# Kernel tuning notes

Measured on AMD Instinct MI355X. Metric: run time of the kernel, lower is better.

Reference implementation:

```python
import jax, jax.numpy as jnp
import numpy as np

N_IN = 100000
N_OUT = 200000
C_IN = 128
C_OUT = 64
K = 27  # 3x3x3 kernel offsets
M = 100000  # neighbor-map pairs per kernel offset
BN_EPS = 1e-5


def setup_inputs() -> dict:
    key = jax.random.key(0)
    k1, k2, k3, k4 = jax.random.split(key, 4)
    x = jax.random.normal(k1, (N_IN, C_IN), dtype=jnp.float32)
    weight = jax.random.normal(k2, (K, C_IN, C_OUT), dtype=jnp.float32) * (1.0 / np.sqrt(C_IN * K))
    gamma = jnp.ones((C_OUT,), dtype=jnp.float32)
    beta = jnp.zeros((C_OUT,), dtype=jnp.float32)
    in_map = jax.random.randint(k3, (K, M), 0, N_IN, dtype=jnp.int32)
    out_map = jax.random.randint(k4, (K, M), 0, N_OUT, dtype=jnp.int32)
    return {"x": x, "weight": weight, "gamma": gamma, "beta": beta,
            "in_map": in_map, "out_map": out_map}


def sparse_transposed_conv(x, weight, in_map, out_map):
    # gather-GEMM-scatter over K kernel offsets (torchsparse semantics)
    out = jnp.zeros((N_OUT, C_OUT), dtype=x.dtype)

    def body(k, out):
        gathered = x[in_map[k]]                # [M, C_in] irregular gather
        contrib = gathered @ weight[k]         # [M, C_out] small GEMM
        return out.at[out_map[k]].add(contrib) # irregular scatter-add

    return jax.lax.fori_loop(0, K, body, out)


def reference(x, weight, gamma, beta, in_map, out_map):
    out = sparse_transposed_conv(x, weight, in_map, out_map)
    # BatchNorm over points (training-mode batch statistics, biased var)
    mean = jnp.mean(out, axis=0)
    var = jnp.mean(jnp.square(out - mean), axis=0)
    y = (out - mean) * (gamma * jax.lax.rsqrt(var + BN_EPS)) + beta
    return jnp.maximum(y, 0.0)  # ReLU
```

## Files before the change

### kernel.cpp

```cpp
#include <hip/hip_runtime.h>
#include <hip/hip_fp16.h>

#define N_IN   100000
#define N_OUT  200000
#define C_IN   128
#define C_OUT  64
#define NK     27
#define MM     100000
#define BN_EPS 1e-5f

#define TILE_M 128
#define APAD   136

typedef short bf16x8 __attribute__((ext_vector_type(8)));
typedef float f32x4  __attribute__((ext_vector_type(4)));

__device__ __forceinline__ unsigned pack2_bf16(float a, float b) {
  unsigned ua = __float_as_uint(a);
  unsigned ub = __float_as_uint(b);
  ua = (ua + 0x7FFFu + ((ua >> 16) & 1u)) >> 16;
  ub = (ub + 0x7FFFu + ((ub >> 16) & 1u)) & 0xFFFF0000u;
  return ua | ub;
}

__device__ __forceinline__ unsigned pack2_f16(float lo, float hi) {
  __half2 h = __floats2half2_rn(lo, hi);
  return *(unsigned*)&h;
}

__device__ __forceinline__ void pk_atomic_f16(const void* addr, unsigned pw) {
  asm volatile("global_atomic_pk_add_f16 %0, %1, off"
               :: "v"((unsigned long long)addr), "v"(pw) : "memory");
}

__global__ void convert_kernel(const float* __restrict__ x, unsigned* __restrict__ xb,
                               const float* __restrict__ w, unsigned* __restrict__ wt) {
  if (blockIdx.x < 6250) {
    int id = blockIdx.x * 256 + threadIdx.x;
    const float4* xs = (const float4*)x;
    float4 v0 = xs[2 * id];
    float4 v1 = xs[2 * id + 1];
    uint4 o;
    o.x = pack2_bf16(v0.x, v0.y);
    o.y = pack2_bf16(v0.z, v0.w);
    o.z = pack2_bf16(v1.x, v1.y);
    o.w = pack2_bf16(v1.z, v1.w);
    ((uint4*)xb)[id] = o;
  } else {
    int pidx = (blockIdx.x - 6250) * 256 + threadIdx.x;
    int k   = pidx >> 12;
    int rem = pidx & 4095;
    int co  = rem >> 6;
    int ci0 = (rem & 63) * 2;
    const float* wk = w + (size_t)k * C_IN * C_OUT;
    float a = wk[ci0 * C_OUT + co];
    float b = wk[(ci0 + 1) * C_OUT + co];
    wt[pidx] = pack2_bf16(a, b);
  }
}

__global__ __launch_bounds__(256, 4) void scatter3_kernel(
    const uint4* __restrict__ xb,
    const unsigned short* __restrict__ wt,
    const int* __restrict__ in_map,
    const int* __restrict__ out_map,
    unsigned short* __restrict__ acc16)
{
  __shared__ unsigned short Bls[C_OUT * APAD];

  const int t = threadIdx.x;
  const int k = blockIdx.y;
  const int mbase = blockIdx.x * TILE_M;

  {
    const uint4* src = (const uint4*)(wt + (size_t)k * C_OUT * C_IN);
    #pragma unroll
    for (int i = 0; i < 4; ++i) {
      int ch  = t + i * 256;
      int co  = ch >> 4;
      int ci0 = (ch & 15) * 8;
      *(uint4*)&Bls[co * APAD + ci0] = src[ch];
    }
  }

  const int wave = t >> 6;
  const int lane = t & 63;
  const int quad = lane >> 4;
  const int l15  = lane & 15;
  const int rb   = wave * 32;

  const int m0 = mbase + rb + l15;
  const int m1 = m0 + 16;
  const int src0 = (m0 < MM) ? in_map[k * MM + m0] : 0;
  const int src1 = (m1 < MM) ? in_map[k * MM + m1] : 0;
  const uint4* xr0 = xb + (size_t)src0 * 16 + quad;
  const uint4* xr1 = xb + (size_t)src1 * 16 + quad;
  uint4 a0[4], a1[4];
  #pragma unroll
  for (int kk = 0; kk < 4; ++kk) {
    a0[kk] = xr0[kk * 4];
    a1[kk] = xr1[kk * 4];
  }

  __syncthreads();

  f32x4 acc[2][4];
  #pragma unroll
  for (int i = 0; i < 2; ++i)
    #pragma unroll
    for (int j = 0; j < 4; ++j)
      acc[i][j] = (f32x4){0.f, 0.f, 0.f, 0.f};

  #pragma unroll
  for (int kk = 0; kk < 4; ++kk) {
    const int koff = kk * 32 + quad * 8;
    bf16x8 fa0 = *(const bf16x8*)&a0[kk];
    bf16x8 fa1 = *(const bf16x8*)&a1[kk];
    bf16x8 b0 = *(const bf16x8*)&Bls[(l15) * APAD + koff];
    bf16x8 b1 = *(const bf16x8*)&Bls[(16 + l15) * APAD + koff];
    bf16x8 b2 = *(const bf16x8*)&Bls[(32 + l15) * APAD + koff];
    bf16x8 b3 = *(const bf16x8*)&Bls[(48 + l15) * APAD + koff];
    acc[0][0] = __builtin_amdgcn_mfma_f32_16x16x32_bf16(fa0, b0, acc[0][0], 0, 0, 0);
    acc[0][1] = __builtin_amdgcn_mfma_f32_16x16x32_bf16(fa0, b1, acc[0][1], 0, 0, 0);
    acc[0][2] = __builtin_amdgcn_mfma_f32_16x16x32_bf16(fa0, b2, acc[0][2], 0, 0, 0);
    acc[0][3] = __builtin_amdgcn_mfma_f32_16x16x32_bf16(fa0, b3, acc[0][3], 0, 0, 0);
    acc[1][0] = __builtin_amdgcn_mfma_f32_16x16x32_bf16(fa1, b0, acc[1][0], 0, 0, 0);
    acc[1][1] = __builtin_amdgcn_mfma_f32_16x16x32_bf16(fa1, b1, acc[1][1], 0, 0, 0);
    acc[1][2] = __builtin_amdgcn_mfma_f32_16x16x32_bf16(fa1, b2, acc[1][2], 0, 0, 0);
    acc[1][3] = __builtin_amdgcn_mfma_f32_16x16x32_bf16(fa1, b3, acc[1][3], 0, 0, 0);
  }

  const int par = l15 & 1;
  #pragma unroll
  for (int rt = 0; rt < 2; ++rt) {
    int rloc = rb + rt * 16 + quad * 4;
    int mrow = mbase + rloc;
    int4 o4;
    if (mrow + 3 < MM) {
      o4 = *(const int4*)(out_map + (size_t)k * MM + mrow);
    } else {
      o4.x = (mrow + 0 < MM) ? out_map[(size_t)k * MM + mrow + 0] : 0;
      o4.y = (mrow + 1 < MM) ? out_map[(size_t)k * MM + mrow + 1] : 0;
      o4.z = (mrow + 2 < MM) ? out_map[(size_t)k * MM + mrow + 2] : 0;
      o4.w = (mrow + 3 < MM) ? out_map[(size_t)k * MM + mrow + 3] : 0;
    }
    int om4[4] = {o4.x, o4.y, o4.z, o4.w};
    #pragma unroll
    for (int ct = 0; ct < 4; ++ct) {
      f32x4 v = acc[rt][ct];
      int colb = ct * 16 + (l15 & ~1);
      #pragma unroll
      for (int i = 0; i < 4; ++i) {
        float vn = __shfl_xor(v[i], 1);
        float lo = par ? vn : v[i];
        float hi = par ? v[i] : vn;
        unsigned pw = pack2_f16(lo, hi);
        if (((i & 1) == par) && (mrow + i < MM)) {
          const unsigned short* addr = acc16 + (size_t)om4[i] * C_OUT + colb;
          pk_atomic_f16(addr, pw);
        }
      }
    }
  }
}

__global__ __launch_bounds__(256) void scatter_f32_kernel(
    const float* __restrict__ x,
    const unsigned short* __restrict__ wt,
    const int* __restrict__ in_map,
    const int* __restrict__ out_map,
    float* __restrict__ outf)
{
  __shared__ unsigned short Als[TILE_M * APAD];
  __shared__ unsigned short Bls[C_OUT * APAD];
  __shared__ int om[TILE_M];

  const int t = threadIdx.x;
  const int k = blockIdx.y;
  const int mbase = blockIdx.x * TILE_M;

  if (t < TILE_M) {
    int m = mbase + t;
    om[t] = (m < MM) ? out_map[k * MM + m] : 0;
  }
  {
    const uint4* src = (const uint4*)(wt + (size_t)k * C_OUT * C_IN);
    #pragma unroll
    for (int i = 0; i < 4; ++i) {
      int ch  = t + i * 256;
      int co  = ch >> 4;
      int ci0 = (ch & 15) * 8;
      *(uint4*)&Bls[co * APAD + ci0] = src[ch];
    }
  }
  {
    int r    = t >> 1;
    int half = t & 1;
    int m    = mbase + r;
    int src  = (m < MM) ? in_map[k * MM + m] : 0;
    const float4* xr = (const float4*)(x + (size_t)src * C_IN) + half * 16;
    uint2* dst = (uint2*)&Als[r * APAD + half * 64];
    #pragma unroll
    for (int j = 0; j < 16; ++j) {
      float4 v = xr[j];
      dst[j] = make_uint2(pack2_bf16(v.x, v.y), pack2_bf16(v.z, v.w));
    }
  }
  __syncthreads();

  const int wave = t >> 6;
  const int lane = t & 63;
  const int quad = lane >> 4;
  const int l15  = lane & 15;
  const int rb   = wave * 32;

  f32x4 acc[2][4];
  #pragma unroll
  for (int i = 0; i < 2; ++i)
    #pragma unroll
    for (int j = 0; j < 4; ++j)
      acc[i][j] = (f32x4){0.f, 0.f, 0.f, 0.f};

  #pragma unroll
  for (int kk = 0; kk < 4; ++kk) {
    const int koff = kk * 32 + quad * 8;
    bf16x8 a0 = *(const bf16x8*)&Als[(rb + l15) * APAD + koff];
    bf16x8 a1 = *(const bf16x8*)&Als[(rb + 16 + l15) * APAD + koff];
    bf16x8 b0 = *(const bf16x8*)&Bls[(l15) * APAD + koff];
    bf16x8 b1 = *(const bf16x8*)&Bls[(16 + l15) * APAD + koff];
    bf16x8 b2 = *(const bf16x8*)&Bls[(32 + l15) * APAD + koff];
    bf16x8 b3 = *(const bf16x8*)&Bls[(48 + l15) * APAD + koff];
    acc[0][0] = __builtin_amdgcn_mfma_f32_16x16x32_bf16(a0, b0, acc[0][0], 0, 0, 0);
    acc[0][1] = __builtin_amdgcn_mfma_f32_16x16x32_bf16(a0, b1, acc[0][1], 0, 0, 0);
    acc[0][2] = __builtin_amdgcn_mfma_f32_16x16x32_bf16(a0, b2, acc[0][2], 0, 0, 0);
    acc[0][3] = __builtin_amdgcn_mfma_f32_16x16x32_bf16(a0, b3, acc[0][3], 0, 0, 0);
    acc[1][0] = __builtin_amdgcn_mfma_f32_16x16x32_bf16(a1, b0, acc[1][0], 0, 0, 0);
    acc[1][1] = __builtin_amdgcn_mfma_f32_16x16x32_bf16(a1, b1, acc[1][1], 0, 0, 0);
    acc[1][2] = __builtin_amdgcn_mfma_f32_16x16x32_bf16(a1, b2, acc[1][2], 0, 0, 0);
    acc[1][3] = __builtin_amdgcn_mfma_f32_16x16x32_bf16(a1, b3, acc[1][3], 0, 0, 0);
  }

  #pragma unroll
  for (int rt = 0; rt < 2; ++rt) {
    int rloc = rb + rt * 16 + quad * 4;
    int4 o4 = *(const int4*)&om[rloc];
    int mrow = mbase + rloc;
    #pragma unroll
    for (int ct = 0; ct < 4; ++ct) {
      f32x4 v = acc[rt][ct];
      int col = ct * 16 + l15;
      if (mrow + 0 < MM) unsafeAtomicAdd(&outf[(size_t)o4.x * C_OUT + col], v[0]);
      if (mrow + 1 < MM) unsafeAtomicAdd(&outf[(size_t)o4.y * C_OUT + col], v[1]);
      if (mrow + 2 < MM) unsafeAtomicAdd(&outf[(size_t)o4.z * C_OUT + col], v[2]);
      if (mrow + 3 < MM) unsafeAtomicAdd(&outf[(size_t)o4.w * C_OUT + col], v[3]);
    }
  }
}

__global__ __launch_bounds__(256) void stats16_kernel(const unsigned* __restrict__ acc,
                                                      float* __restrict__ ws) {
  __shared__ float red[4][8][32];
  int t = threadIdx.x;
  int w = t & 31, sub = t >> 5;
  float s0 = 0, q0 = 0, s1 = 0, q1 = 0;
  for (int r = blockIdx.x * 8 + sub; r < N_OUT; r += gridDim.x * 8) {
    unsigned u = acc[(size_t)r * 32 + w];
    __half2 h = *(__half2*)&u;
    float a = __low2float(h), b = __high2float(h);
    s0 += a; q0 += a * a; s1 += b; q1 += b * b;
  }
  red[0][sub][w] = s0; red[1][sub][w] = q0;
  red[2][sub][w] = s1; red[3][sub][w] = q1;
  __syncthreads();
  if (t < 32) {
    float S0 = 0, Q0 = 0, S1 = 0, Q1 = 0;
    #pragma unroll
    for (int s = 0; s < 8; ++s) {
      S0 += red[0][s][t]; Q0 += red[1][s][t];
      S1 += red[2][s][t]; Q1 += red[3][s][t];
    }
    unsafeAtomicAdd(&ws[2 * t],      S0);
    unsafeAtomicAdd(&ws[64 + 2 * t], Q0);
    unsafeAtomicAdd(&ws[2 * t + 1],      S1);
    unsafeAtomicAdd(&ws[64 + 2 * t + 1], Q1);
  }
}

__global__ void finalize16_kernel(const uint2* __restrict__ acc,
                                  float* __restrict__ out,
                                  const float* __restrict__ ws) {
  int i = blockIdx.x * 256 + threadIdx.x;
  uint2 u = acc[i];
  __half2 h0 = *(__half2*)&u.x;
  __half2 h1 = *(__half2*)&u.y;
  int c0 = (i & 15) * 4;
  float s0 = ws[128 + c0], s1 = ws[129 + c0], s2 = ws[130 + c0], s3 = ws[131 + c0];
  float b0 = ws[192 + c0], b1 = ws[193 + c0], b2 = ws[194 + c0], b3 = ws[195 + c0];
  float4 v;
  v.x = fmaxf(fmaf(__low2float(h0),  s0, b0), 0.f);
  v.y = fmaxf(fmaf(__high2float(h0), s1, b1), 0.f);
  v.z = fmaxf(fmaf(__low2float(h1),  s2, b2), 0.f);
  v.w = fmaxf(fmaf(__high2float(h1), s3, b3), 0.f);
  ((float4*)out)[i] = v;
}

__global__ void stats_kernel(const float* __restrict__ out, float* __restrict__ ws) {
  __shared__ float ls[4][64];
  __shared__ float ls2[4][64];
  int t = threadIdx.x;
  int c = t & 63, sub = t >> 6;
  float s = 0.f, s2 = 0.f;
  for (int r = blockIdx.x * 4 + sub; r < N_OUT; r += gridDim.x * 4) {
    float v = out[(size_t)r * C_OUT + c];
    s += v; s2 += v * v;
  }
  ls[sub][c] = s; ls2[sub][c] = s2;
  __syncthreads();
  if (t < 64) {
    float ts = ls[0][t] + ls[1][t] + ls[2][t] + ls[3][t];
    float t2 = ls2[0][t] + ls2[1][t] + ls2[2][t] + ls2[3][t];
    unsafeAtomicAdd(&ws[t], ts);
    unsafeAtomicAdd(&ws[64 + t], t2);
  }
}

__global__ void finalize_kernel(float* __restrict__ out, const float* __restrict__ ws) {
  int i = blockIdx.x * 256 + threadIdx.x;
  float4 v = ((const float4*)out)[i];
  int c0 = (i & 15) * 4;
  float s0 = ws[128 + c0], s1 = ws[129 + c0], s2 = ws[130 + c0], s3 = ws[131 + c0];
  float b0 = ws[192 + c0], b1 = ws[193 + c0], b2 = ws[194 + c0], b3 = ws[195 + c0];
  v.x = fmaxf(fmaf(v.x, s0, b0), 0.f);
  v.y = fmaxf(fmaf(v.y, s1, b1), 0.f);
  v.z = fmaxf(fmaf(v.z, s2, b2), 0.f);
  v.w = fmaxf(fmaf(v.w, s3, b3), 0.f);
  ((float4*)out)[i] = v;
}

__global__ void prep_kernel(float* __restrict__ ws,
                            const float* __restrict__ gamma,
                            const float* __restrict__ beta) {
  int c = threadIdx.x;
  float mean = ws[c] * (1.0f / N_OUT);
  float var  = ws[64 + c] * (1.0f / N_OUT) - mean * mean;
  var = fmaxf(var, 0.0f);
  float sc = gamma[c] * rsqrtf(var + BN_EPS);
  ws[128 + c] = sc;
  ws[192 + c] = beta[c] - mean * sc;
}

extern "C" void kernel_launch(void* const* d_in, const int* in_sizes, int n_in,
                              void* d_out, int out_size, void* d_ws, size_t ws_size,
                              hipStream_t stream) {
  const float* x      = (const float*)d_in[0];
  const float* weight = (const float*)d_in[1];
  const float* gamma  = (const float*)d_in[2];
  const float* beta   = (const float*)d_in[3];
  const int* in_map   = (const int*)d_in[4];
  const int* out_map  = (const int*)d_in[5];
  float* out   = (float*)d_out;
  float* stats = (float*)d_ws;

  const size_t WT_OFF  = 4096;
  const size_t XB_OFF  = 1u << 20;
  const size_t XB_SZ   = (size_t)N_IN * C_IN * 2;
  const size_t ACC_OFF = XB_OFF + XB_SZ;
  const size_t ACC_SZ  = (size_t)N_OUT * C_OUT * 2;

  unsigned* wt = (unsigned*)((char*)d_ws + WT_OFF);
  unsigned* xb = (unsigned*)((char*)d_ws + XB_OFF);
  unsigned short* acc16 = (unsigned short*)((char*)d_ws + ACC_OFF);

  dim3 g((MM + TILE_M - 1) / TILE_M, NK);
  hipMemsetAsync(d_ws, 0, 1024, stream);

  if (ws_size >= ACC_OFF + ACC_SZ) {
    hipMemsetAsync(acc16, 0, ACC_SZ, stream);
    convert_kernel<<<6682, 256, 0, stream>>>(x, xb, weight, wt);
    scatter3_kernel<<<g, 256, 0, stream>>>((const uint4*)xb, (const unsigned short*)wt,
                                           in_map, out_map, acc16);
    stats16_kernel<<<1024, 256, 0, stream>>>((const unsigned*)acc16, stats);
    prep_kernel<<<1, 64, 0, stream>>>(stats, gamma, beta);
    finalize16_kernel<<<(N_OUT * C_OUT / 4 + 255) / 256, 256, 0, stream>>>(
        (const uint2*)acc16, out, stats);
  } else {
    hipMemsetAsync(d_out, 0, (size_t)N_OUT * C_OUT * sizeof(float), stream);
    convert_kernel<<<6682, 256, 0, stream>>>(x, xb, weight, wt);
    scatter_f32_kernel<<<g, 256, 0, stream>>>(x, (const unsigned short*)wt,
                                              in_map, out_map, out);
    stats_kernel<<<512, 256, 0, stream>>>(out, stats);
    prep_kernel<<<1, 64, 0, stream>>>(stats, gamma, beta);
    finalize_kernel<<<(N_OUT * C_OUT / 4 + 255) / 256, 256, 0, stream>>>(out, stats);
  }
}
```

Before: 732.8 us.

## Replace atomic scatter with bucketed per-output gather reduction of stored contributions

Instead of scattering GEMM results with packed fp16 atomics, the kernel first buckets pair indices by output row using a count/fill pass. It then writes every per-pair contribution densely to a large fp16 buffer and reduces each output row by gathering its bucket entries. Rows with more than CAP pairs fall back to an overflow list fixed with atomics. This removes contended atomics but adds roughly 345MB of contribution writes and reads, a bucket table, and an extra atomic counting pass. Whether the new path runs depends on workspace size.

```diff
diff --git a/kernel.cpp b/kernel.cpp
--- a/kernel.cpp
+++ b/kernel.cpp
@@ -11,6 +11,8 @@
 
 #define TILE_M 128
 #define APAD   136
+#define CAP    64
+#define OVF_CAP 4096
 
 typedef short bf16x8 __attribute__((ext_vector_type(8)));
 typedef float f32x4  __attribute__((ext_vector_type(4)));
@@ -59,12 +61,26 @@
   }
 }
 
-__global__ __launch_bounds__(256, 4) void scatter3_kernel(
+__global__ void count_fill_kernel(const int* __restrict__ out_map,
+                                  int* __restrict__ cnt, int* __restrict__ bucket,
+                                  int* __restrict__ ovfcnt, int* __restrict__ ovf) {
+  int i = blockIdx.x * 256 + threadIdx.x;
+  if (i >= NK * MM) return;
+  int o = out_map[i];
+  int pos = atomicAdd(&cnt[o], 1);
+  if (pos < CAP) {
+    bucket[(size_t)o * CAP + pos] = i;
+  } else {
+    int s = atomicAdd(ovfcnt, 1);
+    if (s < OVF_CAP) ovf[s] = i;
+  }
+}
+
+__global__ __launch_bounds__(256, 8) void contrib_kernel(
     const uint4* __restrict__ xb,
     const unsigned short* __restrict__ wt,
     const int* __restrict__ in_map,
-    const int* __restrict__ out_map,
-    unsigned short* __restrict__ acc16)
+    unsigned* __restrict__ contrib)
 {
   __shared__ unsigned short Bls[C_OUT * APAD];
 
@@ -131,6 +147,196 @@
   }
 
   const int par = l15 & 1;
+  const size_t pbase = (size_t)k * MM;
+  #pragma unroll
+  for (int rt = 0; rt < 2; ++rt) {
+    int mrow = mbase + rb + rt * 16 + quad * 4;
+    #pragma unroll
+    for (int ct = 0; ct < 4; ++ct) {
+      f32x4 v = acc[rt][ct];
+      int ub = ct * 8 + (l15 >> 1);
+      #pragma unroll
+      for (int i = 0; i < 4; ++i) {
+        float vn = __shfl_xor(v[i], 1);
+        float lo = par ? vn : v[i];
+        float hi = par ? v[i] : vn;
+        unsigned pw = pack2_f16(lo, hi);
+        if (((i & 1) == par) && (mrow + i < MM)) {
+          contrib[(pbase + mrow + i) * 32 + ub] = pw;
+        }
+      }
+    }
+  }
+}
+
+__global__ __launch_bounds__(256) void reduce_kernel(
+    const unsigned* __restrict__ contrib,
+    const int* __restrict__ cnt,
+    const int* __restrict__ bucket,
+    float* __restrict__ out)
+{
+  int t = threadIdx.x;
+  int half = t >> 5;
+  int l32  = t & 31;
+  int r = blockIdx.x * 8 + half;
+  int c = cnt[r];
+  c = c > CAP ? CAP : c;
+  const int* bk = bucket + (size_t)r * CAP;
+  float s0 = 0.f, s1 = 0.f;
+  int e = 0;
+  for (; e + 2 <= c; e += 2) {
+    int p0 = bk[e];
+    int p1 = bk[e + 1];
+    unsigned u0 = contrib[(size_t)p0 * 32 + l32];
+    unsigned u1 = contrib[(size_t)p1 * 32 + l32];
+    __half2 h0 = *(__half2*)&u0;
+    __half2 h1 = *(__half2*)&u1;
+    s0 += __low2float(h0) + __low2float(h1);
+    s1 += __high2float(h0) + __high2float(h1);
+  }
+  if (e < c) {
+    int p0 = bk[e];
+    unsigned u0 = contrib[(size_t)p0 * 32 + l32];
+    __half2 h0 = *(__half2*)&u0;
+    s0 += __low2float(h0);
+    s1 += __high2float(h0);
+  }
+  ((float2*)out)[(size_t)r * 32 + l32] = make_float2(s0, s1);
+}
+
+__global__ void ovf_fix_kernel(const int* __restrict__ ovfcnt, const int* __restrict__ ovf,
+                               const unsigned* __restrict__ contrib,
+                               const int* __restrict__ out_map, float* __restrict__ out) {
+  int n = *ovfcnt;
+  n = n > OVF_CAP ? OVF_CAP : n;
+  for (int w = threadIdx.x; w < n * 32; w += 256) {
+    int e = w >> 5, j = w & 31;
+    int pid = ovf[e];
+    int o = out_map[pid];
+    unsigned u = contrib[(size_t)pid * 32 + j];
+    __half2 h = *(__half2*)&u;
+    unsafeAtomicAdd(&out[(size_t)o * C_OUT + 2 * j],     __low2float(h));
+    unsafeAtomicAdd(&out[(size_t)o * C_OUT + 2 * j + 1], __high2float(h));
+  }
+}
+
+__global__ void stats_kernel(const float* __restrict__ out, float* __restrict__ ws) {
+  __shared__ float ls[4][64];
+  __shared__ float ls2[4][64];
+  int t = threadIdx.x;
+  int c = t & 63, sub = t >> 6;
+  float s = 0.f, s2 = 0.f;
+  for (int r = blockIdx.x * 4 + sub; r < N_OUT; r += gridDim.x * 4) {
+    float v = out[(size_t)r * C_OUT + c];
+    s += v; s2 += v * v;
+  }
+  ls[sub][c] = s; ls2[sub][c] = s2;
+  __syncthreads();
+  if (t < 64) {
+    float ts = ls[0][t] + ls[1][t] + ls[2][t] + ls[3][t];
+    float t2 = ls2[0][t] + ls2[1][t] + ls2[2][t] + ls2[3][t];
+    unsafeAtomicAdd(&ws[t], ts);
+    unsafeAtomicAdd(&ws[64 + t], t2);
+  }
+}
+
+__global__ void prep_kernel(float* __restrict__ ws,
+                            const float* __restrict__ gamma,
+                            const float* __restrict__ beta) {
+  int c = threadIdx.x;
+  float mean = ws[c] * (1.0f / N_OUT);
+  float var  = ws[64 + c] * (1.0f / N_OUT) - mean * mean;
+  var = fmaxf(var, 0.0f);
+  float sc = gamma[c] * rsqrtf(var + BN_EPS);
+  ws[128 + c] = sc;
+  ws[192 + c] = beta[c] - mean * sc;
+}
+
+__global__ void finalize_kernel(float* __restrict__ out, const float* __restrict__ ws) {
+  int i = blockIdx.x * 256 + threadIdx.x;
+  float4 v = ((const float4*)out)[i];
+  int c0 = (i & 15) * 4;
+  float s0 = ws[128 + c0], s1 = ws[129 + c0], s2 = ws[130 + c0], s3 = ws[131 + c0];
+  float b0 = ws[192 + c0], b1 = ws[193 + c0], b2 = ws[194 + c0], b3 = ws[195 + c0];
+  v.x = fmaxf(fmaf(v.x, s0, b0), 0.f);
+  v.y = fmaxf(fmaf(v.y, s1, b1), 0.f);
+  v.z = fmaxf(fmaf(v.z, s2, b2), 0.f);
+  v.w = fmaxf(fmaf(v.w, s3, b3), 0.f);
+  ((float4*)out)[i] = v;
+}
+
+__global__ __launch_bounds__(256, 4) void scatter3_kernel(
+    const uint4* __restrict__ xb,
+    const unsigned short* __restrict__ wt,
+    const int* __restrict__ in_map,
+    const int* __restrict__ out_map,
+    unsigned short* __restrict__ acc16)
+{
+  __shared__ unsigned short Bls[C_OUT * APAD];
+
+  const int t = threadIdx.x;
+  const int k = blockIdx.y;
+  const int mbase = blockIdx.x * TILE_M;
+
+  {
+    const uint4* src = (const uint4*)(wt + (size_t)k * C_OUT * C_IN);
+    #pragma unroll
+    for (int i = 0; i < 4; ++i) {
+      int ch  = t + i * 256;
+      int co  = ch >> 4;
+      int ci0 = (ch & 15) * 8;
+      *(uint4*)&Bls[co * APAD + ci0] = src[ch];
+    }
+  }
+
+  const int wave = t >> 6;
+  const int lane = t & 63;
+  const int quad = lane >> 4;
+  const int l15  = lane & 15;
+  const int rb   = wave * 32;
+
+  const int m0 = mbase + rb + l15;
+  const int m1 = m0 + 16;
+  const int src0 = (m0 < MM) ? in_map[k * MM + m0] : 0;
+  const int src1 = (m1 < MM) ? in_map[k * MM + m1] : 0;
+  const uint4* xr0 = xb + (size_t)src0 * 16 + quad;
+  const uint4* xr1 = xb + (size_t)src1 * 16 + quad;
+  uint4 a0[4], a1[4];
+  #pragma unroll
+  for (int kk = 0; kk < 4; ++kk) {
+    a0[kk] = xr0[kk * 4];
+    a1[kk] = xr1[kk * 4];
+  }
+
+  __syncthreads();
+
+  f32x4 acc[2][4];
+  #pragma unroll
+  for (int i = 0; i < 2; ++i)
+    #pragma unroll
+    for (int j = 0; j < 4; ++j)
+      acc[i][j] = (f32x4){0.f, 0.f, 0.f, 0.f};
+
+  #pragma unroll
+  for (int kk = 0; kk < 4; ++kk) {
+    const int koff = kk * 32 + quad * 8;
+    bf16x8 fa0 = *(const bf16x8*)&a0[kk];
+    bf16x8 fa1 = *(const bf16x8*)&a1[kk];
+    bf16x8 b0 = *(const bf16x8*)&Bls[(l15) * APAD + koff];
+    bf16x8 b1 = *(const bf16x8*)&Bls[(16 + l15) * APAD + koff];
+    bf16x8 b2 = *(const bf16x8*)&Bls[(32 + l15) * APAD + koff];
+    bf16x8 b3 = *(const bf16x8*)&Bls[(48 + l15) * APAD + koff];
+    acc[0][0] = __builtin_amdgcn_mfma_f32_16x16x32_bf16(fa0, b0, acc[0][0], 0, 0, 0);
+    acc[0][1] = __builtin_amdgcn_mfma_f32_16x16x32_bf16(fa0, b1, acc[0][1], 0, 0, 0);
+    acc[0][2] = __builtin_amdgcn_mfma_f32_16x16x32_bf16(fa0, b2, acc[0][2], 0, 0, 0);
+    acc[0][3] = __builtin_amdgcn_mfma_f32_16x16x32_bf16(fa0, b3, acc[0][3], 0, 0, 0);
+    acc[1][0] = __builtin_amdgcn_mfma_f32_16x16x32_bf16(fa1, b0, acc[1][0], 0, 0, 0);
+    acc[1][1] = __builtin_amdgcn_mfma_f32_16x16x32_bf16(fa1, b1, acc[1][1], 0, 0, 0);
+    acc[1][2] = __builtin_amdgcn_mfma_f32_16x16x32_bf16(fa1, b2, acc[1][2], 0, 0, 0);
+    acc[1][3] = __builtin_amdgcn_mfma_f32_16x16x32_bf16(fa1, b3, acc[1][3], 0, 0, 0);
+  }
+
+  const int par = l15 & 1;
   #pragma unroll
   for (int rt = 0; rt < 2; ++rt) {
     int rloc = rb + rt * 16 + quad * 4;
@@ -160,99 +366,6 @@
           pk_atomic_f16(addr, pw);
         }
       }
-    }
-  }
-}
-
-__global__ __launch_bounds__(256) void scatter_f32_kernel(
-    const float* __restrict__ x,
-    const unsigned short* __restrict__ wt,
-    const int* __restrict__ in_map,
-    const int* __restrict__ out_map,
-    float* __restrict__ outf)
-{
-  __shared__ unsigned short Als[TILE_M * APAD];
-  __shared__ unsigned short Bls[C_OUT * APAD];
-  __shared__ int om[TILE_M];
-
-  const int t = threadIdx.x;
-  const int k = blockIdx.y;
-  const int mbase = blockIdx.x * TILE_M;
-
-  if (t < TILE_M) {
-    int m = mbase + t;
-    om[t] = (m < MM) ? out_map[k * MM + m] : 0;
-  }
-  {
-    const uint4* src = (const uint4*)(wt + (size_t)k * C_OUT * C_IN);
-    #pragma unroll
-    for (int i = 0; i < 4; ++i) {
-      int ch  = t + i * 256;
-      int co  = ch >> 4;
-      int ci0 = (ch & 15) * 8;
-      *(uint4*)&Bls[co * APAD + ci0] = src[ch];
-    }
-  }
-  {
-    int r    = t >> 1;
-    int half = t & 1;
-    int m    = mbase + r;
-    int src  = (m < MM) ? in_map[k * MM + m] : 0;
-    const float4* xr = (const float4*)(x + (size_t)src * C_IN) + half * 16;
-    uint2* dst = (uint2*)&Als[r * APAD + half * 64];
-    #pragma unroll
-    for (int j = 0; j < 16; ++j) {
-      float4 v = xr[j];
-      dst[j] = make_uint2(pack2_bf16(v.x, v.y), pack2_bf16(v.z, v.w));
-    }
-  }
-  __syncthreads();
-
-  const int wave = t >> 6;
-  const int lane = t & 63;
-  const int quad = lane >> 4;
-  const int l15  = lane & 15;
-  const int rb   = wave * 32;
-
-  f32x4 acc[2][4];
-  #pragma unroll
-  for (int i = 0; i < 2; ++i)
-    #pragma unroll
-    for (int j = 0; j < 4; ++j)
-      acc[i][j] = (f32x4){0.f, 0.f, 0.f, 0.f};
-
-  #pragma unroll
-  for (int kk = 0; kk < 4; ++kk) {
-    const int koff = kk * 32 + quad * 8;
-    bf16x8 a0 = *(const bf16x8*)&Als[(rb + l15) * APAD + koff];
-    bf16x8 a1 = *(const bf16x8*)&Als[(rb + 16 + l15) * APAD + koff];
-    bf16x8 b0 = *(const bf16x8*)&Bls[(l15) * APAD + koff];
-    bf16x8 b1 = *(const bf16x8*)&Bls[(16 + l15) * APAD + koff];
-    bf16x8 b2 = *(const bf16x8*)&Bls[(32 + l15) * APAD + koff];
-    bf16x8 b3 = *(const bf16x8*)&Bls[(48 + l15) * APAD + koff];
-    acc[0][0] = __builtin_amdgcn_mfma_f32_16x16x32_bf16(a0, b0, acc[0][0], 0, 0, 0);
-    acc[0][1] = __builtin_amdgcn_mfma_f32_16x16x32_bf16(a0, b1, acc[0][1], 0, 0, 0);
-    acc[0][2] = __builtin_amdgcn_mfma_f32_16x16x32_bf16(a0, b2, acc[0][2], 0, 0, 0);
-    acc[0][3] = __builtin_amdgcn_mfma_f32_16x16x32_bf16(a0, b3, acc[0][3], 0, 0, 0);
-    acc[1][0] = __builtin_amdgcn_mfma_f32_16x16x32_bf16(a1, b0, acc[1][0], 0, 0, 0);
-    acc[1][1] = __builtin_amdgcn_mfma_f32_16x16x32_bf16(a1, b1, acc[1][1], 0, 0, 0);
-    acc[1][2] = __builtin_amdgcn_mfma_f32_16x16x32_bf16(a1, b2, acc[1][2], 0, 0, 0);
-    acc[1][3] = __builtin_amdgcn_mfma_f32_16x16x32_bf16(a1, b3, acc[1][3], 0, 0, 0);
-  }
-
-  #pragma unroll
-  for (int rt = 0; rt < 2; ++rt) {
-    int rloc = rb + rt * 16 + quad * 4;
-    int4 o4 = *(const int4*)&om[rloc];
-    int mrow = mbase + rloc;
-    #pragma unroll
-    for (int ct = 0; ct < 4; ++ct) {
-      f32x4 v = acc[rt][ct];
-      int col = ct * 16 + l15;
-      if (mrow + 0 < MM) unsafeAtomicAdd(&outf[(size_t)o4.x * C_OUT + col], v[0]);
-      if (mrow + 1 < MM) unsafeAtomicAdd(&outf[(size_t)o4.y * C_OUT + col], v[1]);
-      if (mrow + 2 < MM) unsafeAtomicAdd(&outf[(size_t)o4.z * C_OUT + col], v[2]);
-      if (mrow + 3 < MM) unsafeAtomicAdd(&outf[(size_t)o4.w * C_OUT + col], v[3]);
     }
   }
 }
@@ -304,51 +417,6 @@
   ((float4*)out)[i] = v;
 }
 
-__global__ void stats_kernel(const float* __restrict__ out, float* __restrict__ ws) {
-  __shared__ float ls[4][64];
-  __shared__ float ls2[4][64];
-  int t = threadIdx.x;
-  int c = t & 63, sub = t >> 6;
-  float s = 0.f, s2 = 0.f;
-  for (int r = blockIdx.x * 4 + sub; r < N_OUT; r += gridDim.x * 4) {
-    float v = out[(size_t)r * C_OUT + c];
-    s += v; s2 += v * v;
-  }
-  ls[sub][c] = s; ls2[sub][c] = s2;
-  __syncthreads();
-  if (t < 64) {
-    float ts = ls[0][t] + ls[1][t] + ls[2][t] + ls[3][t];
-    float t2 = ls2[0][t] + ls2[1][t] + ls2[2][t] + ls2[3][t];
-    unsafeAtomicAdd(&ws[t], ts);
-    unsafeAtomicAdd(&ws[64 + t], t2);
-  }
-}
-
-__global__ void finalize_kernel(float* __restrict__ out, const float* __restrict__ ws) {
-  int i = blockIdx.x * 256 + threadIdx.x;
-  float4 v = ((const float4*)out)[i];
-  int c0 = (i & 15) * 4;
-  float s0 = ws[128 + c0], s1 = ws[129 + c0], s2 = ws[130 + c0], s3 = ws[131 + c0];
-  float b0 = ws[192 + c0], b1 = ws[193 + c0], b2 = ws[194 + c0], b3 = ws[195 + c0];
-  v.x = fmaxf(fmaf(v.x, s0, b0), 0.f);
-  v.y = fmaxf(fmaf(v.y, s1, b1), 0.f);
-  v.z = fmaxf(fmaf(v.z, s2, b2), 0.f);
-  v.w = fmaxf(fmaf(v.w, s3, b3), 0.f);
-  ((float4*)out)[i] = v;
-}
-
-__global__ void prep_kernel(float* __restrict__ ws,
-                            const float* __restrict__ gamma,
-                            const float* __restrict__ beta) {
-  int c = threadIdx.x;
-  float mean = ws[c] * (1.0f / N_OUT);
-  float var  = ws[64 + c] * (1.0f / N_OUT) - mean * mean;
-  var = fmaxf(var, 0.0f);
-  float sc = gamma[c] * rsqrtf(var + BN_EPS);
-  ws[128 + c] = sc;
-  ws[192 + c] = beta[c] - mean * sc;
-}
-
 extern "C" void kernel_launch(void* const* d_in, const int* in_sizes, int n_in,
                               void* d_out, int out_size, void* d_ws, size_t ws_size,
                               hipStream_t stream) {
@@ -361,35 +429,51 @@
   float* out   = (float*)d_out;
   float* stats = (float*)d_ws;
 
-  const size_t WT_OFF  = 4096;
-  const size_t XB_OFF  = 1u << 20;
-  const size_t XB_SZ   = (size_t)N_IN * C_IN * 2;
-  const size_t ACC_OFF = XB_OFF + XB_SZ;
-  const size_t ACC_SZ  = (size_t)N_OUT * C_OUT * 2;
-
-  unsigned* wt = (unsigned*)((char*)d_ws + WT_OFF);
-  unsigned* xb = (unsigned*)((char*)d_ws + XB_OFF);
-  unsigned short* acc16 = (unsigned short*)((char*)d_ws + ACC_OFF);
+  const size_t OVFC_OFF   = 1024;
+  const size_t OVF_OFF    = 2048;
+  const size_t CNT_OFF    = 20480;
+  const size_t HEAD_BYTES = CNT_OFF + (size_t)N_OUT * 4;
+  const size_t WT_OFF     = (size_t)1 << 20;
+  const size_t XB_OFF     = (size_t)2 << 20;
+  const size_t XB_SZ      = (size_t)N_IN * C_IN * 2;
+  const size_t BUCKET_OFF = (size_t)28 << 20;
+  const size_t BUCKET_SZ  = (size_t)N_OUT * CAP * 4;
+  const size_t CONTRIB_OFF = (size_t)81 << 20;
+  const size_t CONTRIB_SZ  = (size_t)NK * MM * C_OUT * 2;
+
+  int*      ovfcnt = (int*)((char*)d_ws + OVFC_OFF);
+  int*      ovf    = (int*)((char*)d_ws + OVF_OFF);
+  int*      cnt    = (int*)((char*)d_ws + CNT_OFF);
+  unsigned* wt     = (unsigned*)((char*)d_ws + WT_OFF);
+  unsigned* xb     = (unsigned*)((char*)d_ws + XB_OFF);
+  int*      bucket = (int*)((char*)d_ws + BUCKET_OFF);
+  unsigned* contrib = (unsigned*)((char*)d_ws + CONTRIB_OFF);
 
   dim3 g((MM + TILE_M - 1) / TILE_M, NK);
-  hipMemsetAsync(d_ws, 0, 1024, stream);
-
-  if (ws_size >= ACC_OFF + ACC_SZ) {
+
+  if (ws_size >= CONTRIB_OFF + CONTRIB_SZ) {
+    hipMemsetAsync(d_ws, 0, HEAD_BYTES, stream);
+    convert_kernel<<<6682, 256, 0, stream>>>(x, xb, weight, wt);
+    count_fill_kernel<<<(NK * MM + 255) / 256, 256, 0, stream>>>(out_map, cnt, bucket,
+                                                                 ovfcnt, ovf);
+    contrib_kernel<<<g, 256, 0, stream>>>((const uint4*)xb, (const unsigned short*)wt,
+                                          in_map, contrib);
+    reduce_kernel<<<N_OUT / 8, 256, 0, stream>>>(contrib, cnt, bucket, out);
+    ovf_fix_kernel<<<1, 256, 0, stream>>>(ovfcnt, ovf, contrib, out_map, out);
+    stats_kernel<<<512, 256, 0, stream>>>(out, stats);
+    prep_kernel<<<1, 64, 0, stream>>>(stats, gamma, beta);
+    finalize_kernel<<<(N_OUT * C_OUT / 4) / 256, 256, 0, stream>>>(out, stats);
+  } else {
+    unsigned short* acc16 = (unsigned short*)((char*)d_ws + BUCKET_OFF);
+    const size_t ACC_SZ = (size_t)N_OUT * C_OUT * 2;
+    hipMemsetAsync(d_ws, 0, 1024, stream);
     hipMemsetAsync(acc16, 0, ACC_SZ, stream);
     convert_kernel<<<6682, 256, 0, stream>>>(x, xb, weight, wt);
     scatter3_kernel<<<g, 256, 0, stream>>>((const uint4*)xb, (const unsigned short*)wt,
                                            in_map, out_map, acc16);
     stats16_kernel<<<1024, 256, 0, stream>>>((const unsigned*)acc16, stats);
     prep_kernel<<<1, 64, 0, stream>>>(stats, gamma, beta);
-    finalize16_kernel<<<(N_OUT * C_OUT / 4 + 255) / 256, 256, 0, stream>>>(
+    finalize16_kernel<<<(N_OUT * C_OUT / 4) / 256, 256, 0, stream>>>(
         (const uint2*)acc16, out, stats);
-  } else {
-    hipMemsetAsync(d_out, 0, (size_t)N_OUT * C_OUT * sizeof(float), stream);
-    convert_kernel<<<6682, 256, 0, stream>>>(x, xb, weight, wt);
-    scatter_f32_kernel<<<g, 256, 0, stream>>>(x, (const unsigned short*)wt,
-                                              in_map, out_map, out);
-    stats_kernel<<<512, 256, 0, stream>>>(out, stats);
-    prep_kernel<<<1, 64, 0, stream>>>(stats, gamma, beta);
-    finalize_kernel<<<(N_OUT * C_OUT / 4 + 255) / 256, 256, 0, stream>>>(out, stats);
-  }
-}
+  }
+}
```

Result: no change. 733.4 us (+0.1%).
